# Optimization experiments

Measured on AMD Instinct MI355X. Metric: run time of the kernel, lower is better.

Reference implementation:

```python
import jax, jax.numpy as jnp
import numpy as np

B, H, W, D = 16, 64, 64, 512

def setup_inputs() -> dict:
    key = jax.random.key(0)
    k1, k2, k3, k4, k5, k6 = jax.random.split(key, 6)
    x = jax.random.normal(k1, (B, H, W, D), dtype=jnp.float32)
    attentionXFull = jax.random.normal(k2, (B, H, W, W), dtype=jnp.float32)
    attentionYFull = jax.random.normal(k3, (B, W, H, H), dtype=jnp.float32)
    valueFull = jax.random.normal(k4, (B, H, W, D), dtype=jnp.float32)
    # Learned scalar Gaussian params: shift initialized positive, bias negative
    shift = jnp.abs(jax.random.normal(k5, (1,), dtype=jnp.float32))
    bias = -jnp.abs(jax.random.normal(k6, (1,), dtype=jnp.float32))
    return {"x": x, "attentionXFull": attentionXFull, "attentionYFull": attentionYFull,
            "valueFull": valueFull, "shift": shift, "bias": bias}

def reference(x, attentionXFull, attentionYFull, valueFull, shift, bias):
    # valueFull: [B,H,W,D]; attentionXFull: [B,H,W,W] (last axis = row positions h)
    # attentionYFull: [B,W,H,H] (indexed [b,c,r,w], last axis = col positions w)
    Bv, Hd, Wd, Dd = valueFull.shape
    cw = jnp.arange(Wd, dtype=valueFull.dtype)
    # disX[c,h] = -(shift*(h-c)^2 + bias)
    disX = -(shift[0] * (cw[None, :] - cw[:, None]) ** 2 + bias[0])  # [W,W]
    aX = jax.nn.sigmoid(disX[None, None, :, :] + attentionXFull)     # [B,H,W,W]
    outX = jnp.einsum('brch,brhd->brcd', aX, valueFull)              # row attention
    rh = jnp.arange(Hd, dtype=valueFull.dtype)
    # disY[r,w] = -(shift*(w-r)^2 + bias)
    disY = -(shift[0] * (rh[None, :] - rh[:, None]) ** 2 + bias[0])  # [H,H]
    aY = jax.nn.sigmoid(disY[None, None, :, :] + attentionYFull)     # [B,W,H,H] as [b,c,r,w]
    outY = jnp.einsum('bcrw,bwcd->brcd', aY, valueFull)              # column attention
    return outX + outY
```

## Files before the change

### kernel.cpp

```cpp
#include <hip/hip_runtime.h>
#include <stdint.h>


typedef __attribute__((ext_vector_type(8))) __bf16 bf16x8;
typedef __attribute__((ext_vector_type(8))) short short8;
typedef __attribute__((ext_vector_type(4))) float f32x4;

union U8 { short8 s; bf16x8 b; unsigned short u[8]; };

__device__ __forceinline__ unsigned short f2bf(float f) {
    union { float f; unsigned int i; } v; v.f = f;
    return (unsigned short)((v.i + 0x7fffu + ((v.i >> 16) & 1u)) >> 16);
}
__device__ __forceinline__ float fsigmoid(float x) {
    float e = __builtin_amdgcn_exp2f(-1.44269504f * x);
    return __builtin_amdgcn_rcpf(1.0f + e);
}

template <int S_I, int S_K, bool ACCUM>
__global__ __launch_bounds__(256)
void gauss_gemm(const float* __restrict__ att,
                const float* __restrict__ V,
                float* __restrict__ out,
                const float* __restrict__ shiftp,
                const float* __restrict__ biasp) {
    __shared__ unsigned short S[4096];

    const int bid   = blockIdx.x;
    const int dhalf = bid & 1;
    const int i     = (bid >> 1) & 63;
    const int b     = bid >> 7;
    const int t     = threadIdx.x;

    const float shift = shiftp[0];
    const float bias  = biasp[0];

    const float* ab = att + (size_t)(b * 64 + i) * 4096;
#pragma unroll
    for (int chunk = 0; chunk < 2; ++chunk) {
        int flat = t + chunk * 256;
        int q = flat >> 6, m = flat & 63;
        const float* ap = ab + m * 64 + q * 8;
        f32x4 av0 = *(const f32x4*)(ap);
        f32x4 av1 = *(const f32x4*)(ap + 4);
        U8 res;
#pragma unroll
        for (int j = 0; j < 8; ++j) {
            float a    = (j < 4) ? av0[j & 3] : av1[j & 3];
            float diff = (float)(q * 8 + j - m);
            float dis  = -(shift * diff * diff + bias);
            res.u[j]   = f2bf(fsigmoid(dis + a));
        }
        *(short8*)(&S[flat * 8]) = res.s;
    }
    __syncthreads();

    const int lane = t & 63, wid = t >> 6;
    const int l15 = lane & 15, quad = lane >> 4;
    const int dbase = dhalf * 256 + wid * 64;

    const size_t base = (size_t)b * 2097152 + (size_t)i * S_I;
    const float* vb = V + base;

    f32x4 acc[4][4];
#pragma unroll
    for (int mt = 0; mt < 4; ++mt)
#pragma unroll
        for (int nt = 0; nt < 4; ++nt) acc[mt][nt] = (f32x4)0.0f;

#pragma unroll
    for (int ks = 0; ks < 2; ++ks) {
        bf16x8 af[4];
#pragma unroll
        for (int mt = 0; mt < 4; ++mt) {
            U8 a;
            a.s = *(const short8*)(&S[((ks * 4 + quad) * 64 + mt * 16 + l15) * 8]);
            af[mt] = a.b;
        }
#pragma unroll
        for (int nt = 0; nt < 4; ++nt) {
            const int d = dbase + nt * 16 + l15;
            const float* vp = vb + (size_t)(ks * 32 + quad * 8) * S_K + d;
            U8 bvec;
#pragma unroll
            for (int j = 0; j < 8; ++j) bvec.u[j] = f2bf(vp[(size_t)j * S_K]);
#pragma unroll
            for (int mt = 0; mt < 4; ++mt)
                acc[mt][nt] = __builtin_amdgcn_mfma_f32_16x16x32_bf16(
                    af[mt], bvec.b, acc[mt][nt], 0, 0, 0);
        }
    }

    float* ob = out + base;
#pragma unroll
    for (int mt = 0; mt < 4; ++mt)
#pragma unroll
        for (int nt = 0; nt < 4; ++nt)
#pragma unroll
            for (int reg = 0; reg < 4; ++reg) {
                int m = mt * 16 + quad * 4 + reg;
                int d = dbase + nt * 16 + l15;
                size_t off = (size_t)m * S_K + d;
                float v = acc[mt][nt][reg];
                if (ACCUM) v += ob[off];
                ob[off] = v;
            }
}

extern "C" void kernel_launch(void* const* d_in, const int* in_sizes, int n_in,
                              void* d_out, int out_size, void* d_ws, size_t ws_size,
                              hipStream_t stream) {
    const float* attX = (const float*)d_in[1];
    const float* attY = (const float*)d_in[2];
    const float* V    = (const float*)d_in[3];
    const float* shp  = (const float*)d_in[4];
    const float* bip  = (const float*)d_in[5];
    float* out = (float*)d_out;

    dim3 blk(256);
    dim3 grid(16 * 64 * 2);
    gauss_gemm<32768, 512, false><<<grid, blk, 0, stream>>>(attX, V, out, shp, bip);
    gauss_gemm<512, 32768, true><<<grid, blk, 0, stream>>>(attY, V, out, shp, bip);
}
```

Measured before the change: 445.5 us.

## Stage V tile through LDS transposed as bf16 and split D into quarters

New measurement: 414.5 us. 1.07x faster.

```diff
diff --git a/kernel.cpp b/kernel.cpp
--- a/kernel.cpp
+++ b/kernel.cpp
@@ -5,8 +5,9 @@
 typedef __attribute__((ext_vector_type(8))) __bf16 bf16x8;
 typedef __attribute__((ext_vector_type(8))) short short8;
 typedef __attribute__((ext_vector_type(4))) float f32x4;
+typedef __attribute__((ext_vector_type(4))) unsigned int uint4v;
 
-union U8 { short8 s; bf16x8 b; unsigned short u[8]; };
+union U8 { short8 s; bf16x8 b; unsigned short u[8]; uint4v q; };
 
 __device__ __forceinline__ unsigned short f2bf(float f) {
     union { float f; unsigned int i; } v; v.f = f;
@@ -25,15 +26,19 @@
                 const float* __restrict__ shiftp,
                 const float* __restrict__ biasp) {
     __shared__ unsigned short S[4096];
+    __shared__ unsigned short VT[128 * 66];
 
-    const int bid   = blockIdx.x;
-    const int dhalf = bid & 1;
-    const int i     = (bid >> 1) & 63;
-    const int b     = bid >> 7;
-    const int t     = threadIdx.x;
+    const int bid    = blockIdx.x;
+    const int dq     = bid & 3;
+    const int i      = (bid >> 2) & 63;
+    const int b      = bid >> 8;
+    const int t      = threadIdx.x;
+    const int dstart = dq * 128;
 
     const float shift = shiftp[0];
     const float bias  = biasp[0];
+
+    const size_t base = (size_t)b * 2097152 + (size_t)i * S_I;
 
     const float* ab = att + (size_t)(b * 64 + i) * 4096;
 #pragma unroll
@@ -53,20 +58,30 @@
         }
         *(short8*)(&S[flat * 8]) = res.s;
     }
+
+    {
+        const float* vb = V + base + dstart;
+        const int d4 = t & 31;
+        const int h0 = t >> 5;
+#pragma unroll
+        for (int it = 0; it < 8; ++it) {
+            const int h = h0 + it * 8;
+            f32x4 v = *(const f32x4*)(vb + (size_t)h * S_K + 4 * d4);
+#pragma unroll
+            for (int u = 0; u < 4; ++u)
+                VT[(4 * d4 + u) * 66 + h] = f2bf(v[u]);
+        }
+    }
     __syncthreads();
 
     const int lane = t & 63, wid = t >> 6;
     const int l15 = lane & 15, quad = lane >> 4;
-    const int dbase = dhalf * 256 + wid * 64;
 
-    const size_t base = (size_t)b * 2097152 + (size_t)i * S_I;
-    const float* vb = V + base;
-
-    f32x4 acc[4][4];
+    f32x4 acc[4][2];
 #pragma unroll
     for (int mt = 0; mt < 4; ++mt)
 #pragma unroll
-        for (int nt = 0; nt < 4; ++nt) acc[mt][nt] = (f32x4)0.0f;
+        for (int nt = 0; nt < 2; ++nt) acc[mt][nt] = (f32x4)0.0f;
 
 #pragma unroll
     for (int ks = 0; ks < 2; ++ks) {
@@ -77,13 +92,16 @@
             a.s = *(const short8*)(&S[((ks * 4 + quad) * 64 + mt * 16 + l15) * 8]);
             af[mt] = a.b;
         }
+        const int h = ks * 32 + quad * 8;
 #pragma unroll
-        for (int nt = 0; nt < 4; ++nt) {
-            const int d = dbase + nt * 16 + l15;
-            const float* vp = vb + (size_t)(ks * 32 + quad * 8) * S_K + d;
+        for (int nt = 0; nt < 2; ++nt) {
+            const int dloc = wid * 32 + nt * 16 + l15;
+            const unsigned short* vp = &VT[dloc * 66 + h];
             U8 bvec;
+            uint4v qv;
 #pragma unroll
-            for (int j = 0; j < 8; ++j) bvec.u[j] = f2bf(vp[(size_t)j * S_K]);
+            for (int u = 0; u < 4; ++u) qv[u] = *(const unsigned int*)(vp + 2 * u);
+            bvec.q = qv;
 #pragma unroll
             for (int mt = 0; mt < 4; ++mt)
                 acc[mt][nt] = __builtin_amdgcn_mfma_f32_16x16x32_bf16(
@@ -91,15 +109,15 @@
         }
     }
 
-    float* ob = out + base;
+    float* ob = out + base + dstart;
 #pragma unroll
     for (int mt = 0; mt < 4; ++mt)
 #pragma unroll
-        for (int nt = 0; nt < 4; ++nt)
+        for (int nt = 0; nt < 2; ++nt)
 #pragma unroll
             for (int reg = 0; reg < 4; ++reg) {
                 int m = mt * 16 + quad * 4 + reg;
-                int d = dbase + nt * 16 + l15;
+                int d = wid * 32 + nt * 16 + l15;
                 size_t off = (size_t)m * S_K + d;
                 float v = acc[mt][nt][reg];
                 if (ACCUM) v += ob[off];
@@ -118,7 +136,7 @@
     float* out = (float*)d_out;
 
     dim3 blk(256);
-    dim3 grid(16 * 64 * 2);
+    dim3 grid(16 * 64 * 4);
     gauss_gemm<32768, 512, false><<<grid, blk, 0, stream>>>(attX, V, out, shp, bip);
     gauss_gemm<512, 32768, true><<<grid, blk, 0, stream>>>(attY, V, out, shp, bip);
 }
```
